# Optimization experiments

Hardware: AMD Instinct MI355X
Metric: run time of the kernel (lower is better)

The kernel has to match this reference:

```python
import jax, jax.numpy as jnp
import numpy as np

NEG_SLOPE = 0.01  # torch LeakyReLU default
BN_EPS = 1e-5     # torch BatchNorm1d default


def _bn(x, g, b):
    # training-mode batch norm over the node axis
    m = jnp.mean(x, axis=0)
    v = jnp.var(x, axis=0)
    return g * (x - m) * jax.lax.rsqrt(v + BN_EPS) + b


def _lrelu(x):
    return jax.nn.leaky_relu(x, NEG_SLOPE)


def setup_inputs() -> dict:
    key = jax.random.key(0)
    N, E, W, D = 100_000, 1_600_000, 32, 10
    ks = iter(jax.random.split(key, 64))

    def w(shape):
        fan_in = shape[-2] if len(shape) >= 2 else shape[-1]
        return (jax.random.normal(next(ks), shape, jnp.float32) / np.sqrt(fan_in)).astype(jnp.float32)

    inp = {}
    inp["x"] = jax.random.normal(next(ks), (N, 1), jnp.float32)
    inp["col_e_idx"] = jax.random.randint(next(ks), (2, E), 0, N, dtype=jnp.int32)
    # init_node_feature_trans: MLP 1 -> [32] -> 32, LeakyReLU, batch_norm=True
    inp["Wi0"] = w((1, W)); inp["bi0"] = jnp.zeros(W); inp["gi0"] = jnp.ones(W); inp["bei0"] = jnp.zeros(W)
    inp["Wi1"] = w((W, W)); inp["bi1"] = jnp.zeros(W); inp["gi1"] = jnp.ones(W); inp["bei1"] = jnp.zeros(W)
    # 10 CollConv layers (identical dims -> stacked params)
    inp["Wm"] = w((D, W, W)); inp["bm"] = jnp.zeros((D, W)); inp["gm"] = jnp.ones((D, W)); inp["bem"] = jnp.zeros((D, W))
    inp["Wu"] = w((D, 2 * W, W)); inp["bu"] = jnp.zeros((D, W)); inp["gu"] = jnp.ones((D, W)); inp["beu"] = jnp.zeros((D, W))
    # final_mlp: 32 -> 256 -> 128 -> 64 -> 32 (LeakyReLU, no BN), then 32 -> 1 sigmoid
    inp["Wf0"] = w((W, 256)); inp["bf0"] = jnp.zeros(256)
    inp["Wf1"] = w((256, 128)); inp["bf1"] = jnp.zeros(128)
    inp["Wf2"] = w((128, 64)); inp["bf2"] = jnp.zeros(64)
    inp["Wf3"] = w((64, W)); inp["bf3"] = jnp.zeros(W)
    inp["Wo"] = w((W, 1)); inp["bo"] = jnp.zeros(1)
    return inp


def reference(x, col_e_idx, Wi0, bi0, gi0, bei0, Wi1, bi1, gi1, bei1,
              Wm, bm, gm, bem, Wu, bu, gu, beu,
              Wf0, bf0, Wf1, bf1, Wf2, bf2, Wf3, bf3, Wo, bo):
    N = x.shape[0]
    D = Wm.shape[0]
    src, dst = col_e_idx[0], col_e_idx[1]

    # init node-feature MLP (Linear -> BN -> LeakyReLU, twice)
    h = _lrelu(_bn(x @ Wi0 + bi0, gi0, bei0))
    h = _lrelu(_bn(h @ Wi1 + bi1, gi1, bei1))

    feats = [h]  # middle_features[0]
    for i in range(D):  # fixed small depth -> python loop is fine
        # CollConv: node-wise message transform, edge gather, scatter-sum, update
        msg = _lrelu(_bn(h @ Wm[i] + bm[i], gm[i], bem[i]))      # [N, W]
        agg = jax.ops.segment_sum(msg[src], dst, num_segments=N)  # [N, W]
        h = _lrelu(_bn(jnp.concatenate([h, agg], axis=-1) @ Wu[i] + bu[i], gu[i], beu[i]))
        if i - 2 >= 0:  # residual_skip_num = 2
            h = h + feats[i - 2]
        feats.append(h)

    # final MLP (no BN) + sigmoid head
    h = _lrelu(h @ Wf0 + bf0)
    h = _lrelu(h @ Wf1 + bf1)
    h = _lrelu(h @ Wf2 + bf2)
    h = _lrelu(h @ Wf3 + bf3)
    return jax.nn.sigmoid(h @ Wo + bo)  # [N, 1]
```

## Files before the change

### kernel.cpp

```cpp
#include <hip/hip_runtime.h>
#include <hip/hip_bf16.h>

#define NN 100000
#define NEDGE 1600000
#define NV (NN*32)
#define NEG 0.01f
#define EPS 1e-5f
#define NBLK 391
#define NBKT 391
#define CHUNK 4096
#define NCBLK 391
#define DCAP 6144
#define STC 64
#define ST_STRIDE 4096
#define NGBLK 1563
#define NTILE 3125

#define OFF_STATS 0
#define STATS_F  (22*ST_STRIDE)
#define OFF_PA   STATS_F
#define OFF_PB   (OFF_PA + NV)
#define OFF_TACT (OFF_PB + NV)
#define OFF_MSGB (OFF_TACT + NV)
#define OFF_RING (OFF_MSGB + NV/2)
#define OFF_WF   (OFF_RING + 4*NV)
#define ARENA_F  (OFF_WF + 25600)

#define W0B 0
#define W1B 1024
#define W2B 5120
#define W3B 6144

__device__ __align__(16) float gA[ARENA_F];
__device__ int g_rowptr[NN + 1];
__device__ int g_csr[NEDGE];
__device__ int g_bin[NEDGE];
__device__ int g_bcnt[NBKT];
__device__ int g_boff[NBKT];
__device__ int g_btail[NBKT];

__device__ __forceinline__ float lrelu(float v) { return v > 0.f ? v : v * NEG; }
__device__ __forceinline__ unsigned short f2b(float v) {
    __hip_bfloat16 b = __float2bfloat16(v);
    return *reinterpret_cast<unsigned short*>(&b);
}
__device__ __forceinline__ float b2f(unsigned short u) {
    __hip_bfloat16 b = *reinterpret_cast<__hip_bfloat16*>(&u);
    return __bfloat162float(b);
}

__global__ void k_zero_v19()
{
    int i = blockIdx.x * 256 + threadIdx.x;
    if (i < STATS_F) gA[i] = 0.f;
    if (i < NBKT) g_bcnt[i] = 0;
}

__global__ __launch_bounds__(256) void k_bcnt_v19(const int* __restrict__ col)
{
    __shared__ int hist[NBKT];
    int tid = threadIdx.x;
    for (int b = tid; b < NBKT; b += 256) hist[b] = 0;
    __syncthreads();
    int e0 = blockIdx.x * CHUNK;
    #pragma unroll
    for (int r = 0; r < CHUNK / 256; ++r) {
        int e = e0 + r * 256 + tid;
        if (e < NEDGE) atomicAdd(&hist[col[NEDGE + e] >> 8], 1);
    }
    __syncthreads();
    for (int b = tid; b < NBKT; b += 256) {
        int v = hist[b];
        if (v) atomicAdd(&g_bcnt[b], v);
    }
}

__global__ __launch_bounds__(512) void k_bscan_v19()
{
    __shared__ int s[512];
    int t = threadIdx.x;
    int v = (t < NBKT) ? g_bcnt[t] : 0;
    s[t] = v;
    __syncthreads();
    for (int off = 1; off < 512; off <<= 1) {
        int u = (t >= off) ? s[t - off] : 0;
        __syncthreads();
        s[t] += u;
        __syncthreads();
    }
    if (t < NBKT) {
        int o = s[t] - v;
        g_boff[t] = o;
        g_btail[t] = o;
    }
}

__global__ __launch_bounds__(256) void k_binfill_v19(const int* __restrict__ col)
{
    __shared__ int ssrc[CHUNK];
    __shared__ int sdst[CHUNK];
    __shared__ int hist[NBKT];
    __shared__ int boffL[NBKT];
    __shared__ int cnt2[NBKT];
    int tid = threadIdx.x;
    for (int b = tid; b < NBKT; b += 256) { hist[b] = 0; cnt2[b] = 0; }
    __syncthreads();
    int e0 = blockIdx.x * CHUNK;
    #pragma unroll
    for (int r = 0; r < CHUNK / 256; ++r) {
        int i = r * 256 + tid;
        int e = e0 + i;
        if (e < NEDGE) {
            int s = col[e];
            int d = col[NEDGE + e];
            ssrc[i] = s;
            sdst[i] = d;
            atomicAdd(&hist[d >> 8], 1);
        }
    }
    __syncthreads();
    for (int b = tid; b < NBKT; b += 256) {
        int h = hist[b];
        if (h) boffL[b] = atomicAdd(&g_btail[b], h);
    }
    __syncthreads();
    #pragma unroll
    for (int r = 0; r < CHUNK / 256; ++r) {
        int i = r * 256 + tid;
        int e = e0 + i;
        if (e < NEDGE) {
            int d = sdst[i];
            int b = d >> 8;
            int rk = atomicAdd(&cnt2[b], 1);
            g_bin[boffL[b] + rk] = (ssrc[i] << 8) | (d & 255);
        }
    }
}

__global__ __launch_bounds__(256) void k_csr_v24()
{
    __shared__ int stg[DCAP];
    __shared__ int c1[1024];
    __shared__ int sgb[1024];
    __shared__ int c2[1024];
    __shared__ int sc[256];
    __shared__ int sl[256];
    int tid = threadIdx.x, b = blockIdx.x;
    int base = g_boff[b];
    int cntE = g_bcnt[b];
    #pragma unroll
    for (int k = 0; k < 4; ++k) { c1[tid + 256 * k] = 0; c2[tid + 256 * k] = 0; }
    __syncthreads();
    for (int i = tid; i < cntE; i += 256) {
        int p = g_bin[base + i];
        if (i < DCAP) stg[i] = p;
        atomicAdd(&c1[((p & 255) << 2) | (p >> 23)], 1);
    }
    __syncthreads();
    int t0 = c1[tid * 4], t1 = c1[tid * 4 + 1], t2 = c1[tid * 4 + 2], t3 = c1[tid * 4 + 3];
    int deg = t0 + t1 + t2 + t3;
    sgb[tid * 4]     = 0;
    sgb[tid * 4 + 1] = t0;
    sgb[tid * 4 + 2] = t0 + t1;
    sgb[tid * 4 + 3] = t0 + t1 + t2;
    sc[tid] = deg;
    __syncthreads();
    for (int off = 1; off < 256; off <<= 1) {
        int u = (tid >= off) ? sc[tid - off] : 0;
        __syncthreads();
        sc[tid] += u;
        __syncthreads();
    }
    int loff = sc[tid] - deg;
    sl[tid] = loff;
    int node = b * 256 + tid;
    if (node < NN) g_rowptr[node] = base + loff;
    if (b == NBKT - 1 && tid == 0) g_rowptr[NN] = NEDGE;
    __syncthreads();
    for (int i = tid; i < cntE; i += 256) {
        int p = (i < DCAP) ? stg[i] : g_bin[base + i];
        int dl = p & 255;
        int k2 = (dl << 2) | (p >> 23);
        int rk = atomicAdd(&c2[k2], 1);
        g_csr[base + sl[dl] + sgb[k2] + rk] = p >> 8;
    }
}

__global__ void k_init0_v17(const float* __restrict__ x, const float* __restrict__ Wi0,
                            const float* __restrict__ bi0)
{
    int j = threadIdx.x & 31, ns = threadIdx.x >> 5;
    float w = Wi0[j];
    float bb = bi0[j];
    __shared__ float red[64];
    if (threadIdx.x < 64) red[threadIdx.x] = 0.f;
    __syncthreads();
    float s1 = 0.f, s2 = 0.f;
    for (int t = blockIdx.x; t < NN / 8; t += gridDim.x) {
        int n = t * 8 + ns;
        float v = x[n] * w + bb;
        gA[OFF_PA + n * 32 + j] = v;
        s1 += v; s2 += v * v;
    }
    atomicAdd(&red[j], s1);
    atomicAdd(&red[j + 32], s2);
    __syncthreads();
    if (threadIdx.x < 64)
        atomicAdd(&gA[OFF_STATS + (blockIdx.x & (STC - 1)) * 64 + threadIdx.x], red[threadIdx.x]);
}

__global__ __launch_bounds__(256) void k_nl_v24(int off_in, int off_out, int out_msg, int st_in,
                         const float* __restrict__ gamma, const float* __restrict__ beta,
                         int off_resid, int off_feats,
                         const float* __restrict__ Wn, const float* __restrict__ bn,
                         int st_out)
{
    int tid = threadIdx.x;
    int j = tid & 31, grp = tid >> 5;
    __shared__ float sstat[64];
    __shared__ float red[64];
    __shared__ float sH[32][32];
    if (tid < 64) {
        red[tid] = 0.f;
        float acc = 0.f;
        int base = st_in + tid;
        #pragma unroll 8
        for (int c = 0; c < STC; ++c) acc += gA[base + c * 64];
        sstat[tid] = acc;
    }
    __syncthreads();
    float mean = sstat[j] * (1.f / NN);
    float var  = sstat[32 + j] * (1.f / NN) - mean * mean;
    float scale = gamma[j] * rsqrtf(var + EPS);
    float shift = beta[j] - mean * scale;

    float wc[32]; float bb = 0.f;
    if (Wn) {
        #pragma unroll
        for (int k = 0; k < 32; ++k) wc[k] = Wn[k * 32 + j];
        bb = bn[j];
    }
    unsigned short* mb = (unsigned short*)(gA + OFF_MSGB);
    float s1 = 0.f, s2 = 0.f;
    for (int t = blockIdx.x; t < NTILE; t += gridDim.x) {
        int base = t * 1024;
        #pragma unroll
        for (int k = 0; k < 4; ++k) {
            int idx = tid + 256 * k;
            float v = gA[off_in + base + idx];
            v = lrelu(scale * v + shift);
            if (off_resid >= 0) v += gA[off_resid + base + idx];
            if (off_feats >= 0) gA[off_feats + base + idx] = v;
            ((float*)sH)[idx] = v;
        }
        if (Wn) {
            __syncthreads();
            #pragma unroll
            for (int q = 0; q < 4; ++q) {
                int nl = grp * 4 + q;
                float acc = bb;
                #pragma unroll
                for (int k = 0; k < 32; k += 4) {
                    float4 h4 = *(const float4*)&sH[nl][k];
                    acc += h4.x * wc[k] + h4.y * wc[k + 1] + h4.z * wc[k + 2] + h4.w * wc[k + 3];
                }
                int n = t * 32 + nl;
                if (out_msg) mb[n * 32 + j] = f2b(acc);
                else gA[off_out + n * 32 + j] = acc;
                s1 += acc; s2 += acc * acc;
            }
            __syncthreads();
        }
    }
    if (Wn) {
        atomicAdd(&red[j], s1);
        atomicAdd(&red[j + 32], s2);
        __syncthreads();
        if (tid < 64)
            atomicAdd(&gA[st_out + (blockIdx.x & (STC - 1)) * 64 + tid], red[tid]);
    }
}

__global__ __launch_bounds__(256) void k_act_v21(int st_msg,
                                                 const float* __restrict__ gm,
                                                 const float* __restrict__ bem)
{
    __shared__ float sstat[64];
    __shared__ float scl[32], shf[32];
    int tid = threadIdx.x;
    if (tid < 64) {
        float acc = 0.f;
        int base = st_msg + tid;
        #pragma unroll 8
        for (int c = 0; c < STC; ++c) acc += gA[base + c * 64];
        sstat[tid] = acc;
    }
    __syncthreads();
    if (tid < 32) {
        float mean = sstat[tid] * (1.f / NN);
        float var  = sstat[32 + tid] * (1.f / NN) - mean * mean;
        float s = gm[tid] * rsqrtf(var + EPS);
        scl[tid] = s;
        shf[tid] = bem[tid] - mean * s;
    }
    __syncthreads();
    int idx = blockIdx.x * 256 + tid;
    if (idx >= NV / 8) return;
    const uint4* src = (const uint4*)(gA + OFF_MSGB);
    uint4* dst = (uint4*)(gA + OFF_TACT);
    uint4 m = src[idx];
    int fb = (idx & 3) * 8;
    uint4 o;
    #pragma unroll
    for (int w = 0; w < 4; ++w) {
        unsigned int u = (&m.x)[w];
        int f0 = fb + 2 * w;
        float vlo = lrelu(scl[f0]     * __uint_as_float(u << 16)         + shf[f0]);
        float vhi = lrelu(scl[f0 + 1] * __uint_as_float(u & 0xffff0000u) + shf[f0 + 1]);
        (&o.x)[w] = (unsigned int)f2b(vlo) | ((unsigned int)f2b(vhi) << 16);
    }
    dst[idx] = o;
}

__global__ __launch_bounds__(256) void k_gupd_v24(int off_h,
                                                  const float* __restrict__ Wu_i,
                                                  const float* __restrict__ bu_i,
                                                  int st_out)
{
    __shared__ float sH[64][36];
    __shared__ float sAgg[64][36];
    __shared__ float red[64];
    int tid = threadIdx.x;
    int nb = blockIdx.x * 64;

    if (tid < 64) red[tid] = 0.f;
    {
        const float* hp = gA + off_h + nb * 32;
        int lim = min(2048, (NN - nb) * 32);
        for (int idx = tid; idx < lim; idx += 256)
            sH[idx >> 5][idx & 31] = hp[idx];
    }

    {
        int nl = tid >> 2;
        int g  = tid & 3;
        int n  = nb + nl;
        float a[8];
        #pragma unroll
        for (int q = 0; q < 8; ++q) a[q] = 0.f;
        if (n < NN) {
            const unsigned short* tb = (const unsigned short*)(gA + OFF_TACT);
            int e0 = g_rowptr[n], e1 = g_rowptr[n + 1];
            int e = e0;
            for (; e + 3 < e1; e += 4) {
                int sg = g_csr[e + g];
                int s0 = __shfl(sg, 0, 4);
                int s1 = __shfl(sg, 1, 4);
                int s2 = __shfl(sg, 2, 4);
                int s3 = __shfl(sg, 3, 4);
                uint4 m0 = *(const uint4*)(tb + (s0 << 5) + (g << 3));
                uint4 m1 = *(const uint4*)(tb + (s1 << 5) + (g << 3));
                uint4 m2 = *(const uint4*)(tb + (s2 << 5) + (g << 3));
                uint4 m3 = *(const uint4*)(tb + (s3 << 5) + (g << 3));
                #pragma unroll
                for (int w = 0; w < 4; ++w) {
                    unsigned int u0 = (&m0.x)[w], u1 = (&m1.x)[w], u2 = (&m2.x)[w], u3 = (&m3.x)[w];
                    int q = w * 2;
                    a[q]   += __uint_as_float(u0 << 16) + __uint_as_float(u1 << 16)
                            + __uint_as_float(u2 << 16) + __uint_as_float(u3 << 16);
                    a[q+1] += __uint_as_float(u0 & 0xffff0000u) + __uint_as_float(u1 & 0xffff0000u)
                            + __uint_as_float(u2 & 0xffff0000u) + __uint_as_float(u3 & 0xffff0000u);
                }
            }
            for (; e < e1; ++e) {
                int s0 = g_csr[e];
                uint4 m0 = *(const uint4*)(tb + (s0 << 5) + (g << 3));
                #pragma unroll
                for (int w = 0; w < 4; ++w) {
                    unsigned int u0 = (&m0.x)[w];
                    int q = w * 2;
                    a[q]   += __uint_as_float(u0 << 16);
                    a[q+1] += __uint_as_float(u0 & 0xffff0000u);
                }
            }
        }
        *(float4*)&sAgg[nl][g * 8]     = make_float4(a[0], a[1], a[2], a[3]);
        *(float4*)&sAgg[nl][g * 8 + 4] = make_float4(a[4], a[5], a[6], a[7]);
    }
    __syncthreads();

    {
        int j = tid & 31, ns = tid >> 5;
        float wc[64];
        #pragma unroll
        for (int k = 0; k < 64; ++k) wc[k] = Wu_i[k * 32 + j];
        float bb = bu_i[j];
        float s1 = 0.f, s2 = 0.f;
        #pragma unroll
        for (int it = 0; it < 8; ++it) {
            int nl = it * 8 + ns;
            int n = nb + nl;
            if (n >= NN) break;
            float acc = bb;
            #pragma unroll
            for (int k = 0; k < 32; k += 4) {
                float4 h4 = *(const float4*)&sH[nl][k];
                acc += h4.x * wc[k] + h4.y * wc[k + 1] + h4.z * wc[k + 2] + h4.w * wc[k + 3];
                float4 a4 = *(const float4*)&sAgg[nl][k];
                acc += a4.x * wc[32 + k] + a4.y * wc[32 + k + 1] + a4.z * wc[32 + k + 2] + a4.w * wc[32 + k + 3];
            }
            gA[OFF_PB + n * 32 + j] = acc;
            s1 += acc; s2 += acc * acc;
        }
        atomicAdd(&red[j], s1);
        atomicAdd(&red[j + 32], s2);
        __syncthreads();
        if (tid < 64)
            atomicAdd(&gA[st_out + (blockIdx.x & (STC - 1)) * 64 + tid], red[tid]);
    }
}

typedef __attribute__((ext_vector_type(8))) short bf16x8;
typedef __attribute__((ext_vector_type(4))) float f32x4;

union FC { uint4 u; bf16x8 b; };

#define MFMA(a, b, c) __builtin_amdgcn_mfma_f32_16x16x32_bf16(a, b, c, 0, 0, 0)

__device__ __forceinline__ bf16x8 ld_wf(const uint4* p) {
    FC c; c.u = *p; return c.b;
}

__device__ __forceinline__ f32x4 ld_bias4(const float* p) {
    float4 t = *(const float4*)p;
    f32x4 r; r[0] = t.x; r[1] = t.y; r[2] = t.z; r[3] = t.w; return r;
}

__device__ __forceinline__ f32x4 lrelu4(f32x4 v) {
    f32x4 r;
    #pragma unroll
    for (int k = 0; k < 4; ++k) r[k] = v[k] > 0.f ? v[k] : v[k] * NEG;
    return r;
}

__device__ __forceinline__ void splitpack(const float* v, bf16x8& hi, bf16x8& lo) {
    unsigned int h[4], l[4];
    #pragma unroll
    for (int k = 0; k < 4; ++k) {
        unsigned short h0 = f2b(v[2*k]), h1 = f2b(v[2*k+1]);
        float r0 = v[2*k]   - b2f(h0);
        float r1 = v[2*k+1] - b2f(h1);
        h[k] = (unsigned int)h0 | ((unsigned int)h1 << 16);
        l[k] = (unsigned int)f2b(r0) | ((unsigned int)f2b(r1) << 16);
    }
    FC ch; ch.u = make_uint4(h[0], h[1], h[2], h[3]); hi = ch.b;
    FC cl; cl.u = make_uint4(l[0], l[1], l[2], l[3]); lo = cl.b;
}

__global__ __launch_bounds__(256) void k_wprep_v18(const float* __restrict__ W0,
                                                   const float* __restrict__ W1,
                                                   const float* __restrict__ W2,
                                                   const float* __restrict__ W3)
{
    int i = blockIdx.x * 256 + threadIdx.x;
    if (i >= 51200) return;
    const float* src; int Nout, nk; int r = i;
    if (r < 8192)       { src = W0; Nout = 256; nk = 1; }
    else if (r < 40960) { src = W1; Nout = 128; nk = 8; r -= 8192; }
    else if (r < 49152) { src = W2; Nout = 64;  nk = 4; r -= 40960; }
    else                { src = W3; Nout = 32;  nk = 2; r -= 49152; }
    int frag = r >> 9;
    int lane = (r >> 3) & 63;
    int j = r & 7;
    int T = frag / nk, s = frag - T * nk;
    int g = lane >> 4;
    int outf = T * 16 + (lane & 15);
    int inf = 32 * s + 16 * (j >> 2) + 4 * g + (j & 3);
    unsigned short* dst = (unsigned short*)(gA + OFF_WF);
    dst[i] = f2b(src[inf * Nout + outf]);
}

__global__ __launch_bounds__(256) void k_final_v18(
    int off_h,
    const float* __restrict__ bf0, const float* __restrict__ bf1,
    const float* __restrict__ bf2, const float* __restrict__ bf3,
    const float* __restrict__ Wo,  const float* __restrict__ bo,
    float* __restrict__ out)
{
    int lane = threadIdx.x & 63;
    int wave = threadIdx.x >> 6;
    int c = lane & 15;
    int g = lane >> 4;
    int nb = blockIdx.x * 128 + wave * 32;
    int n0 = nb + c;
    int n1 = nb + 16 + c;
    int ld0 = min(n0, NN - 1), ld1 = min(n1, NN - 1);

    const float* h = gA + off_h;
    const uint4* WF = (const uint4*)(gA + OFF_WF);

    float4 ia0 = *(const float4*)&h[ld0 * 32 + 4 * g];
    float4 ib0 = *(const float4*)&h[ld0 * 32 + 16 + 4 * g];
    float4 ia1 = *(const float4*)&h[ld1 * 32 + 4 * g];
    float4 ib1 = *(const float4*)&h[ld1 * 32 + 16 + 4 * g];
    bf16x8 Bh0, Bl0, Bh1, Bl1;
    {
        float v0[8] = {ia0.x, ia0.y, ia0.z, ia0.w, ib0.x, ib0.y, ib0.z, ib0.w};
        float v1[8] = {ia1.x, ia1.y, ia1.z, ia1.w, ib1.x, ib1.y, ib1.z, ib1.w};
        splitpack(v0, Bh0, Bl0);
        splitpack(v1, Bh1, Bl1);
    }

    f32x4 A0[16][2];
    #pragma unroll
    for (int t = 0; t < 16; ++t) {
        f32x4 ci = ld_bias4(bf0 + t * 16 + 4 * g);
        bf16x8 w = ld_wf(WF + W0B + t * 64 + lane);
        f32x4 d0 = MFMA(w, Bh0, ci);
        d0 = MFMA(w, Bl0, d0);
        f32x4 d1 = MFMA(w, Bh1, ci);
        d1 = MFMA(w, Bl1, d1);
        A0[t][0] = lrelu4(d0);
        A0[t][1] = lrelu4(d1);
    }

    f32x4 A1[8][2];
    #pragma unroll
    for (int T = 0; T < 8; ++T) {
        f32x4 ci = ld_bias4(bf1 + T * 16 + 4 * g);
        A1[T][0] = ci; A1[T][1] = ci;
    }
    #pragma unroll
    for (int s = 0; s < 8; ++s) {
        bf16x8 bh[2], bl[2];
        #pragma unroll
        for (int u = 0; u < 2; ++u) {
            float vv[8] = {A0[2*s][u][0], A0[2*s][u][1], A0[2*s][u][2], A0[2*s][u][3],
                           A0[2*s+1][u][0], A0[2*s+1][u][1], A0[2*s+1][u][2], A0[2*s+1][u][3]};
            splitpack(vv, bh[u], bl[u]);
        }
        #pragma unroll
        for (int T = 0; T < 8; ++T) {
            bf16x8 w = ld_wf(WF + W1B + (T * 8 + s) * 64 + lane);
            A1[T][0] = MFMA(w, bh[0], A1[T][0]);
            A1[T][0] = MFMA(w, bl[0], A1[T][0]);
            A1[T][1] = MFMA(w, bh[1], A1[T][1]);
            A1[T][1] = MFMA(w, bl[1], A1[T][1]);
        }
    }
    #pragma unroll
    for (int T = 0; T < 8; ++T) { A1[T][0] = lrelu4(A1[T][0]); A1[T][1] = lrelu4(A1[T][1]); }

    f32x4 A2[4][2];
    #pragma unroll
    for (int T = 0; T < 4; ++T) {
        f32x4 ci = ld_bias4(bf2 + T * 16 + 4 * g);
        A2[T][0] = ci; A2[T][1] = ci;
    }
    #pragma unroll
    for (int s = 0; s < 4; ++s) {
        bf16x8 bh[2], bl[2];
        #pragma unroll
        for (int u = 0; u < 2; ++u) {
            float vv[8] = {A1[2*s][u][0], A1[2*s][u][1], A1[2*s][u][2], A1[2*s][u][3],
                           A1[2*s+1][u][0], A1[2*s+1][u][1], A1[2*s+1][u][2], A1[2*s+1][u][3]};
            splitpack(vv, bh[u], bl[u]);
        }
        #pragma unroll
        for (int T = 0; T < 4; ++T) {
            bf16x8 w = ld_wf(WF + W2B + (T * 4 + s) * 64 + lane);
            A2[T][0] = MFMA(w, bh[0], A2[T][0]);
            A2[T][0] = MFMA(w, bl[0], A2[T][0]);
            A2[T][1] = MFMA(w, bh[1], A2[T][1]);
            A2[T][1] = MFMA(w, bl[1], A2[T][1]);
        }
    }
    #pragma unroll
    for (int T = 0; T < 4; ++T) { A2[T][0] = lrelu4(A2[T][0]); A2[T][1] = lrelu4(A2[T][1]); }

    f32x4 A3[2][2];
    #pragma unroll
    for (int T = 0; T < 2; ++T) {
        f32x4 ci = ld_bias4(bf3 + T * 16 + 4 * g);
        A3[T][0] = ci; A3[T][1] = ci;
    }
    #pragma unroll
    for (int s = 0; s < 2; ++s) {
        bf16x8 bh[2], bl[2];
        #pragma unroll
        for (int u = 0; u < 2; ++u) {
            float vv[8] = {A2[2*s][u][0], A2[2*s][u][1], A2[2*s][u][2], A2[2*s][u][3],
                           A2[2*s+1][u][0], A2[2*s+1][u][1], A2[2*s+1][u][2], A2[2*s+1][u][3]};
            splitpack(vv, bh[u], bl[u]);
        }
        #pragma unroll
        for (int T = 0; T < 2; ++T) {
            bf16x8 w = ld_wf(WF + W3B + (T * 2 + s) * 64 + lane);
            A3[T][0] = MFMA(w, bh[0], A3[T][0]);
            A3[T][0] = MFMA(w, bl[0], A3[T][0]);
            A3[T][1] = MFMA(w, bh[1], A3[T][1]);
            A3[T][1] = MFMA(w, bl[1], A3[T][1]);
        }
    }
    #pragma unroll
    for (int T = 0; T < 2; ++T) { A3[T][0] = lrelu4(A3[T][0]); A3[T][1] = lrelu4(A3[T][1]); }

    float4 woa = *(const float4*)&Wo[4 * g];
    float4 wob = *(const float4*)&Wo[16 + 4 * g];
    float z0 = A3[0][0][0]*woa.x + A3[0][0][1]*woa.y + A3[0][0][2]*woa.z + A3[0][0][3]*woa.w
             + A3[1][0][0]*wob.x + A3[1][0][1]*wob.y + A3[1][0][2]*wob.z + A3[1][0][3]*wob.w;
    float z1 = A3[0][1][0]*woa.x + A3[0][1][1]*woa.y + A3[0][1][2]*woa.z + A3[0][1][3]*woa.w
             + A3[1][1][0]*wob.x + A3[1][1][1]*wob.y + A3[1][1][2]*wob.z + A3[1][1][3]*wob.w;
    z0 += __shfl_xor(z0, 16); z0 += __shfl_xor(z0, 32);
    z1 += __shfl_xor(z1, 16); z1 += __shfl_xor(z1, 32);
    float bb = bo[0];
    if (g == 0 && n0 < NN) out[n0] = 1.f / (1.f + __expf(-(z0 + bb)));
    if (g == 1 && n1 < NN) out[n1] = 1.f / (1.f + __expf(-(z1 + bb)));
}

extern "C" void kernel_launch(void* const* d_in, const int* in_sizes, int n_in,
                              void* d_out, int out_size, void* d_ws, size_t ws_size,
                              hipStream_t stream)
{
    (void)in_sizes; (void)n_in; (void)out_size; (void)d_ws; (void)ws_size;
    float* out = (float*)d_out;

    const float* x   = (const float*)d_in[0];
    const int*  col  = (const int*) d_in[1];
    const float* Wi0 = (const float*)d_in[2];
    const float* bi0 = (const float*)d_in[3];
    const float* gi0 = (const float*)d_in[4];
    const float* bei0= (const float*)d_in[5];
    const float* Wi1 = (const float*)d_in[6];
    const float* bi1 = (const float*)d_in[7];
    const float* gi1 = (const float*)d_in[8];
    const float* bei1= (const float*)d_in[9];
    const float* Wm  = (const float*)d_in[10];
    const float* bm  = (const float*)d_in[11];
    const float* gm  = (const float*)d_in[12];
    const float* bem = (const float*)d_in[13];
    const float* Wu  = (const float*)d_in[14];
    const float* bu  = (const float*)d_in[15];
    const float* gu  = (const float*)d_in[16];
    const float* beu = (const float*)d_in[17];
    const float* Wf0 = (const float*)d_in[18];
    const float* bf0 = (const float*)d_in[19];
    const float* Wf1 = (const float*)d_in[20];
    const float* bf1 = (const float*)d_in[21];
    const float* Wf2 = (const float*)d_in[22];
    const float* bf2 = (const float*)d_in[23];
    const float* Wf3 = (const float*)d_in[24];
    const float* bf3 = (const float*)d_in[25];
    const float* Wo  = (const float*)d_in[26];
    const float* bo  = (const float*)d_in[27];

    const int st_i0 = OFF_STATS;
    const int st_i1 = OFF_STATS + ST_STRIDE;
    const int st_m  = OFF_STATS + 2 * ST_STRIDE;
    const int st_u  = OFF_STATS + 12 * ST_STRIDE;

    const int RING[4] = { OFF_RING, OFF_RING + NV, OFF_RING + 2 * NV, OFF_RING + 3 * NV };

    dim3 blk(256);
    k_zero_v19<<<NBLK, blk, 0, stream>>>();
    k_bcnt_v19<<<NCBLK, blk, 0, stream>>>(col);
    k_bscan_v19<<<1, 512, 0, stream>>>();
    k_binfill_v19<<<NCBLK, blk, 0, stream>>>(col);
    k_csr_v24<<<NBKT, blk, 0, stream>>>();
    k_wprep_v18<<<200, blk, 0, stream>>>(Wf0, Wf1, Wf2, Wf3);

    k_init0_v17<<<1024, blk, 0, stream>>>(x, Wi0, bi0);
    k_nl_v24<<<782, blk, 0, stream>>>(OFF_PA, OFF_PB, 0, st_i0, gi0, bei0, -1, -1, Wi1, bi1, st_i1);
    k_nl_v24<<<782, blk, 0, stream>>>(OFF_PB, 0, 1, st_i1, gi1, bei1, -1, RING[0], Wm, bm, st_m);

    for (int i = 0; i < 10; ++i) {
        int h_cur = RING[i & 3];
        int h_new = RING[(i + 1) & 3];
        int resid = (i >= 2) ? RING[(i - 2) & 3] : -1;
        k_act_v21<<<1563, blk, 0, stream>>>(st_m + i * ST_STRIDE, gm + i * 32, bem + i * 32);
        k_gupd_v24<<<NGBLK, blk, 0, stream>>>(h_cur, Wu + i * 2048, bu + i * 32,
                                              st_u + i * ST_STRIDE);
        const float* Wn = (i < 9) ? (Wm + (i + 1) * 1024) : nullptr;
        const float* bn = (i < 9) ? (bm + (i + 1) * 32) : nullptr;
        int st_next = (i < 9) ? (st_m + (i + 1) * ST_STRIDE) : 0;
        k_nl_v24<<<782, blk, 0, stream>>>(OFF_PB, 0, 1, st_u + i * ST_STRIDE,
                                          gu + i * 32, beu + i * 32,
                                          resid, h_new, Wn, bn, st_next);
    }

    k_final_v18<<<782, blk, 0, stream>>>(RING[2], bf0, bf1, bf2, bf3, Wo, bo, out);
}
```

Baseline: 979.1 us.

## Split activated bf16 messages into two feature planes for gather locality

The activation kernel now writes the bf16 message tensor as two planes of 16 features per node (32 bytes each) instead of one 64-byte row per node. The gather-aggregate kernel makes two passes over each node's edges, one per plane, with 8-byte loads per lane instead of 16-byte loads. The aim is a smaller per-plane working set that fits cache better during the random gather. In exchange the CSR indices are read twice and each plane pass issues more, smaller memory requests.

Result: slower. 1.061 ms (+8.4%).

```diff
diff --git a/kernel.cpp b/kernel.cpp
--- a/kernel.cpp
+++ b/kernel.cpp
@@ -15,6 +15,7 @@
 #define ST_STRIDE 4096
 #define NGBLK 1563
 #define NTILE 3125
+#define PLANE_SH (NN*16)
 
 #define OFF_STATS 0
 #define STATS_F  (22*ST_STRIDE)
@@ -281,7 +282,7 @@
     }
 }
 
-__global__ __launch_bounds__(256) void k_act_v21(int st_msg,
+__global__ __launch_bounds__(256) void k_act_v25(int st_msg,
                                                  const float* __restrict__ gm,
                                                  const float* __restrict__ bem)
 {
@@ -309,7 +310,9 @@
     const uint4* src = (const uint4*)(gA + OFF_MSGB);
     uint4* dst = (uint4*)(gA + OFF_TACT);
     uint4 m = src[idx];
-    int fb = (idx & 3) * 8;
+    int q = idx & 3;
+    int node = idx >> 2;
+    int fb = q * 8;
     uint4 o;
     #pragma unroll
     for (int w = 0; w < 4; ++w) {
@@ -319,10 +322,11 @@
         float vhi = lrelu(scl[f0 + 1] * __uint_as_float(u & 0xffff0000u) + shf[f0 + 1]);
         (&o.x)[w] = (unsigned int)f2b(vlo) | ((unsigned int)f2b(vhi) << 16);
     }
-    dst[idx] = o;
-}
-
-__global__ __launch_bounds__(256) void k_gupd_v24(int off_h,
+    int di = node * 2 + (q & 1) + ((q >> 1) ? (NN * 2) : 0);
+    dst[di] = o;
+}
+
+__global__ __launch_bounds__(256) void k_gupd_v25(int off_h,
                                                   const float* __restrict__ Wu_i,
                                                   const float* __restrict__ bu_i,
                                                   int st_out)
@@ -349,43 +353,48 @@
         #pragma unroll
         for (int q = 0; q < 8; ++q) a[q] = 0.f;
         if (n < NN) {
-            const unsigned short* tb = (const unsigned short*)(gA + OFF_TACT);
             int e0 = g_rowptr[n], e1 = g_rowptr[n + 1];
-            int e = e0;
-            for (; e + 3 < e1; e += 4) {
-                int sg = g_csr[e + g];
-                int s0 = __shfl(sg, 0, 4);
-                int s1 = __shfl(sg, 1, 4);
-                int s2 = __shfl(sg, 2, 4);
-                int s3 = __shfl(sg, 3, 4);
-                uint4 m0 = *(const uint4*)(tb + (s0 << 5) + (g << 3));
-                uint4 m1 = *(const uint4*)(tb + (s1 << 5) + (g << 3));
-                uint4 m2 = *(const uint4*)(tb + (s2 << 5) + (g << 3));
-                uint4 m3 = *(const uint4*)(tb + (s3 << 5) + (g << 3));
-                #pragma unroll
-                for (int w = 0; w < 4; ++w) {
-                    unsigned int u0 = (&m0.x)[w], u1 = (&m1.x)[w], u2 = (&m2.x)[w], u3 = (&m3.x)[w];
-                    int q = w * 2;
-                    a[q]   += __uint_as_float(u0 << 16) + __uint_as_float(u1 << 16)
-                            + __uint_as_float(u2 << 16) + __uint_as_float(u3 << 16);
-                    a[q+1] += __uint_as_float(u0 & 0xffff0000u) + __uint_as_float(u1 & 0xffff0000u)
-                            + __uint_as_float(u2 & 0xffff0000u) + __uint_as_float(u3 & 0xffff0000u);
+            const unsigned short* tb0 = (const unsigned short*)(gA + OFF_TACT);
+            #pragma unroll
+            for (int p = 0; p < 2; ++p) {
+                const unsigned short* tb = tb0 + p * PLANE_SH;
+                float a0 = 0.f, a1 = 0.f, a2 = 0.f, a3 = 0.f;
+                int e = e0;
+                for (; e + 3 < e1; e += 4) {
+                    int sg = g_csr[e + g];
+                    int s0 = __shfl(sg, 0, 4);
+                    int s1 = __shfl(sg, 1, 4);
+                    int s2 = __shfl(sg, 2, 4);
+                    int s3 = __shfl(sg, 3, 4);
+                    uint2 m0 = *(const uint2*)(tb + (s0 << 4) + (g << 2));
+                    uint2 m1 = *(const uint2*)(tb + (s1 << 4) + (g << 2));
+                    uint2 m2 = *(const uint2*)(tb + (s2 << 4) + (g << 2));
+                    uint2 m3 = *(const uint2*)(tb + (s3 << 4) + (g << 2));
+                    a0 += __uint_as_float(m0.x << 16) + __uint_as_float(m1.x << 16)
+                        + __uint_as_float(m2.x << 16) + __uint_as_float(m3.x << 16);
+                    a1 += __uint_as_float(m0.x & 0xffff0000u) + __uint_as_float(m1.x & 0xffff0000u)
+                        + __uint_as_float(m2.x & 0xffff0000u) + __uint_as_float(m3.x & 0xffff0000u);
+                    a2 += __uint_as_float(m0.y << 16) + __uint_as_float(m1.y << 16)
+                        + __uint_as_float(m2.y << 16) + __uint_as_float(m3.y << 16);
+                    a3 += __uint_as_float(m0.y & 0xffff0000u) + __uint_as_float(m1.y & 0xffff0000u)
+                        + __uint_as_float(m2.y & 0xffff0000u) + __uint_as_float(m3.y & 0xffff0000u);
                 }
+                for (; e < e1; ++e) {
+                    int s0 = g_csr[e];
+                    uint2 m0 = *(const uint2*)(tb + (s0 << 4) + (g << 2));
+                    a0 += __uint_as_float(m0.x << 16);
+                    a1 += __uint_as_float(m0.x & 0xffff0000u);
+                    a2 += __uint_as_float(m0.y << 16);
+                    a3 += __uint_as_float(m0.y & 0xffff0000u);
+                }
+                a[p * 4]     = a0;
+                a[p * 4 + 1] = a1;
+                a[p * 4 + 2] = a2;
+                a[p * 4 + 3] = a3;
             }
-            for (; e < e1; ++e) {
-                int s0 = g_csr[e];
-                uint4 m0 = *(const uint4*)(tb + (s0 << 5) + (g << 3));
-                #pragma unroll
-                for (int w = 0; w < 4; ++w) {
-                    unsigned int u0 = (&m0.x)[w];
-                    int q = w * 2;
-                    a[q]   += __uint_as_float(u0 << 16);
-                    a[q+1] += __uint_as_float(u0 & 0xffff0000u);
-                }
-            }
-        }
-        *(float4*)&sAgg[nl][g * 8]     = make_float4(a[0], a[1], a[2], a[3]);
-        *(float4*)&sAgg[nl][g * 8 + 4] = make_float4(a[4], a[5], a[6], a[7]);
+        }
+        *(float4*)&sAgg[nl][g * 4]      = make_float4(a[0], a[1], a[2], a[3]);
+        *(float4*)&sAgg[nl][16 + g * 4] = make_float4(a[4], a[5], a[6], a[7]);
     }
     __syncthreads();
 
@@ -677,8 +686,8 @@
         int h_cur = RING[i & 3];
         int h_new = RING[(i + 1) & 3];
         int resid = (i >= 2) ? RING[(i - 2) & 3] : -1;
-        k_act_v21<<<1563, blk, 0, stream>>>(st_m + i * ST_STRIDE, gm + i * 32, bem + i * 32);
-        k_gupd_v24<<<NGBLK, blk, 0, stream>>>(h_cur, Wu + i * 2048, bu + i * 32,
+        k_act_v25<<<1563, blk, 0, stream>>>(st_m + i * ST_STRIDE, gm + i * 32, bem + i * 32);
+        k_gupd_v25<<<NGBLK, blk, 0, stream>>>(h_cur, Wu + i * 2048, bu + i * 32,
                                               st_u + i * ST_STRIDE);
         const float* Wn = (i < 9) ? (Wm + (i + 1) * 1024) : nullptr;
         const float* bn = (i < 9) ? (bm + (i + 1) * 32) : nullptr;
```

## Pad CSR rows to multiples of four and gather with vectorized index loads

Applied to the files above, without the earlier changes.

The CSR builder pads each node's edge list up to a multiple of four, filling the extra slots with a sentinel node index. It also stores per-node row ends. The aggregation loop can then load source indices as int4 without lane shuffles, unroll eight gathers per iteration, and drop the scalar tail. The goal is more memory-level parallelism and fewer index-load instructions on the dominant gather, at the cost of a few dummy gathers per node. Correctness relies on the sentinel row in the bf16 activation buffer reading as zero.

Result: faster. 932.7 us (-4.7%).

```diff
diff --git a/kernel.cpp b/kernel.cpp
--- a/kernel.cpp
+++ b/kernel.cpp
@@ -15,6 +15,7 @@
 #define ST_STRIDE 4096
 #define NGBLK 1563
 #define NTILE 3125
+#define CSRX (NEDGE + 302080)
 
 #define OFF_STATS 0
 #define STATS_F  (22*ST_STRIDE)
@@ -33,7 +34,8 @@
 
 __device__ __align__(16) float gA[ARENA_F];
 __device__ int g_rowptr[NN + 1];
-__device__ int g_csr[NEDGE];
+__device__ int g_rowend[NN];
+__device__ __align__(16) int g_csr[CSRX];
 __device__ int g_bin[NEDGE];
 __device__ int g_bcnt[NBKT];
 __device__ int g_boff[NBKT];
@@ -137,7 +139,7 @@
     }
 }
 
-__global__ __launch_bounds__(256) void k_csr_v24()
+__global__ __launch_bounds__(256) void k_csr_v27()
 {
     __shared__ int stg[DCAP];
     __shared__ int c1[1024];
@@ -148,6 +150,7 @@
     int tid = threadIdx.x, b = blockIdx.x;
     int base = g_boff[b];
     int cntE = g_bcnt[b];
+    int padbase = ((base + 3) & ~3) + 772 * b;
     #pragma unroll
     for (int k = 0; k < 4; ++k) { c1[tid + 256 * k] = 0; c2[tid + 256 * k] = 0; }
     __syncthreads();
@@ -159,11 +162,12 @@
     __syncthreads();
     int t0 = c1[tid * 4], t1 = c1[tid * 4 + 1], t2 = c1[tid * 4 + 2], t3 = c1[tid * 4 + 3];
     int deg = t0 + t1 + t2 + t3;
+    int pdeg = (deg + 3) & ~3;
     sgb[tid * 4]     = 0;
     sgb[tid * 4 + 1] = t0;
     sgb[tid * 4 + 2] = t0 + t1;
     sgb[tid * 4 + 3] = t0 + t1 + t2;
-    sc[tid] = deg;
+    sc[tid] = pdeg;
     __syncthreads();
     for (int off = 1; off < 256; off <<= 1) {
         int u = (tid >= off) ? sc[tid - off] : 0;
@@ -171,10 +175,13 @@
         sc[tid] += u;
         __syncthreads();
     }
-    int loff = sc[tid] - deg;
+    int loff = sc[tid] - pdeg;
     sl[tid] = loff;
     int node = b * 256 + tid;
-    if (node < NN) g_rowptr[node] = base + loff;
+    if (node < NN) {
+        g_rowptr[node] = padbase + loff;
+        g_rowend[node] = padbase + loff + pdeg;
+    }
     if (b == NBKT - 1 && tid == 0) g_rowptr[NN] = NEDGE;
     __syncthreads();
     for (int i = tid; i < cntE; i += 256) {
@@ -182,7 +189,11 @@
         int dl = p & 255;
         int k2 = (dl << 2) | (p >> 23);
         int rk = atomicAdd(&c2[k2], 1);
-        g_csr[base + sl[dl] + sgb[k2] + rk] = p >> 8;
+        g_csr[padbase + sl[dl] + sgb[k2] + rk] = p >> 8;
+    }
+    if (node < NN) {
+        for (int k = deg; k < pdeg; ++k)
+            g_csr[padbase + loff + k] = NN;
     }
 }
 
@@ -322,7 +333,14 @@
     dst[idx] = o;
 }
 
-__global__ __launch_bounds__(256) void k_gupd_v24(int off_h,
+#define ACC8(mm) { \
+    unsigned int u_; \
+    u_ = (mm).x; a[0] += __uint_as_float(u_ << 16); a[1] += __uint_as_float(u_ & 0xffff0000u); \
+    u_ = (mm).y; a[2] += __uint_as_float(u_ << 16); a[3] += __uint_as_float(u_ & 0xffff0000u); \
+    u_ = (mm).z; a[4] += __uint_as_float(u_ << 16); a[5] += __uint_as_float(u_ & 0xffff0000u); \
+    u_ = (mm).w; a[6] += __uint_as_float(u_ << 16); a[7] += __uint_as_float(u_ & 0xffff0000u); }
+
+__global__ __launch_bounds__(256) void k_gupd_v27(int off_h,
                                                   const float* __restrict__ Wu_i,
                                                   const float* __restrict__ bu_i,
                                                   int st_out)
@@ -350,38 +368,28 @@
         for (int q = 0; q < 8; ++q) a[q] = 0.f;
         if (n < NN) {
             const unsigned short* tb = (const unsigned short*)(gA + OFF_TACT);
-            int e0 = g_rowptr[n], e1 = g_rowptr[n + 1];
-            int e = e0;
-            for (; e + 3 < e1; e += 4) {
-                int sg = g_csr[e + g];
-                int s0 = __shfl(sg, 0, 4);
-                int s1 = __shfl(sg, 1, 4);
-                int s2 = __shfl(sg, 2, 4);
-                int s3 = __shfl(sg, 3, 4);
-                uint4 m0 = *(const uint4*)(tb + (s0 << 5) + (g << 3));
-                uint4 m1 = *(const uint4*)(tb + (s1 << 5) + (g << 3));
-                uint4 m2 = *(const uint4*)(tb + (s2 << 5) + (g << 3));
-                uint4 m3 = *(const uint4*)(tb + (s3 << 5) + (g << 3));
-                #pragma unroll
-                for (int w = 0; w < 4; ++w) {
-                    unsigned int u0 = (&m0.x)[w], u1 = (&m1.x)[w], u2 = (&m2.x)[w], u3 = (&m3.x)[w];
-                    int q = w * 2;
-                    a[q]   += __uint_as_float(u0 << 16) + __uint_as_float(u1 << 16)
-                            + __uint_as_float(u2 << 16) + __uint_as_float(u3 << 16);
-                    a[q+1] += __uint_as_float(u0 & 0xffff0000u) + __uint_as_float(u1 & 0xffff0000u)
-                            + __uint_as_float(u2 & 0xffff0000u) + __uint_as_float(u3 & 0xffff0000u);
-                }
+            int e = g_rowptr[n], e1 = g_rowend[n];
+            for (; e + 7 < e1; e += 8) {
+                int4 c0 = *(const int4*)(g_csr + e);
+                int4 c1 = *(const int4*)(g_csr + e + 4);
+                uint4 m0 = *(const uint4*)(tb + (c0.x << 5) + (g << 3));
+                uint4 m1 = *(const uint4*)(tb + (c0.y << 5) + (g << 3));
+                uint4 m2 = *(const uint4*)(tb + (c0.z << 5) + (g << 3));
+                uint4 m3 = *(const uint4*)(tb + (c0.w << 5) + (g << 3));
+                uint4 m4 = *(const uint4*)(tb + (c1.x << 5) + (g << 3));
+                uint4 m5 = *(const uint4*)(tb + (c1.y << 5) + (g << 3));
+                uint4 m6 = *(const uint4*)(tb + (c1.z << 5) + (g << 3));
+                uint4 m7 = *(const uint4*)(tb + (c1.w << 5) + (g << 3));
+                ACC8(m0) ACC8(m1) ACC8(m2) ACC8(m3)
+                ACC8(m4) ACC8(m5) ACC8(m6) ACC8(m7)
             }
-            for (; e < e1; ++e) {
-                int s0 = g_csr[e];
-                uint4 m0 = *(const uint4*)(tb + (s0 << 5) + (g << 3));
-                #pragma unroll
-                for (int w = 0; w < 4; ++w) {
-                    unsigned int u0 = (&m0.x)[w];
-                    int q = w * 2;
-                    a[q]   += __uint_as_float(u0 << 16);
-                    a[q+1] += __uint_as_float(u0 & 0xffff0000u);
-                }
+            if (e < e1) {
+                int4 c0 = *(const int4*)(g_csr + e);
+                uint4 m0 = *(const uint4*)(tb + (c0.x << 5) + (g << 3));
+                uint4 m1 = *(const uint4*)(tb + (c0.y << 5) + (g << 3));
+                uint4 m2 = *(const uint4*)(tb + (c0.z << 5) + (g << 3));
+                uint4 m3 = *(const uint4*)(tb + (c0.w << 5) + (g << 3));
+                ACC8(m0) ACC8(m1) ACC8(m2) ACC8(m3)
             }
         }
         *(float4*)&sAgg[nl][g * 8]     = make_float4(a[0], a[1], a[2], a[3]);
@@ -666,7 +674,7 @@
     k_bcnt_v19<<<NCBLK, blk, 0, stream>>>(col);
     k_bscan_v19<<<1, 512, 0, stream>>>();
     k_binfill_v19<<<NCBLK, blk, 0, stream>>>(col);
-    k_csr_v24<<<NBKT, blk, 0, stream>>>();
+    k_csr_v27<<<NBKT, blk, 0, stream>>>();
     k_wprep_v18<<<200, blk, 0, stream>>>(Wf0, Wf1, Wf2, Wf3);
 
     k_init0_v17<<<1024, blk, 0, stream>>>(x, Wi0, bi0);
@@ -678,7 +686,7 @@
         int h_new = RING[(i + 1) & 3];
         int resid = (i >= 2) ? RING[(i - 2) & 3] : -1;
         k_act_v21<<<1563, blk, 0, stream>>>(st_m + i * ST_STRIDE, gm + i * 32, bem + i * 32);
-        k_gupd_v24<<<NGBLK, blk, 0, stream>>>(h_cur, Wu + i * 2048, bu + i * 32,
+        k_gupd_v27<<<NGBLK, blk, 0, stream>>>(h_cur, Wu + i * 2048, bu + i * 32,
                                               st_u + i * ST_STRIDE);
         const float* Wn = (i < 9) ? (Wm + (i + 1) * 1024) : nullptr;
         const float* bn = (i < 9) ? (bm + (i + 1) * 32) : nullptr;
```
